# Optimization experiments

Hardware: AMD Instinct MI355X
Metric: run time of the kernel (lower is better)

Reference implementation:

```python
import jax, jax.numpy as jnp
import numpy as np

D_MODEL = 1024
NUM_HEADS = 16
D_K = D_MODEL // NUM_HEADS
B, S = 2, 2048
NEG = -1e9


def setup_inputs() -> dict:
    key = jax.random.key(0)
    ks = jax.random.split(key, 12)
    sc = 1.0 / np.sqrt(D_MODEL)
    inp = {
        'Q': jax.random.normal(ks[0], (B, S, D_MODEL), jnp.float32),
        'K': jax.random.normal(ks[1], (B, S, D_MODEL), jnp.float32),
        'V': jax.random.normal(ks[2], (B, S, D_MODEL), jnp.float32),
        # causal additive mask: 1.0 above diagonal -> scores += mask * -1e9
        'mask': jnp.triu(jnp.ones((S, S), jnp.float32), k=1),
        'Wq': jax.random.normal(ks[3], (D_MODEL, D_MODEL), jnp.float32) * sc,
        'bq': jnp.zeros((D_MODEL,), jnp.float32),
        'Wk': jax.random.normal(ks[4], (D_MODEL, D_MODEL), jnp.float32) * sc,
        'bk': jnp.zeros((D_MODEL,), jnp.float32),
        'Wv': jax.random.normal(ks[5], (D_MODEL, D_MODEL), jnp.float32) * sc,
        'bv': jnp.zeros((D_MODEL,), jnp.float32),
        'Wo': jax.random.normal(ks[6], (D_MODEL, D_MODEL), jnp.float32) * sc,
        'bo': jnp.zeros((D_MODEL,), jnp.float32),
    }
    return inp


def _split_heads(x):
    # [B,S,D] -> [B,H,S,d_k]
    b, s, _ = x.shape
    return x.reshape(b, s, NUM_HEADS, D_K).transpose(0, 2, 1, 3)


def reference(Q, K, V, mask, Wq, bq, Wk, bk, Wv, bv, Wo, bo):
    # torch Linear: y = x @ W.T + b
    q = _split_heads(Q @ Wq.T + bq)  # [B,H,S,d_k]
    k = _split_heads(K @ Wk.T + bk)
    v = _split_heads(V @ Wv.T + bv)
    scores = jnp.einsum('bhqd,bhkd->bhqk', q, k) / np.sqrt(D_K)
    scores = scores + mask * NEG  # mask broadcasts over [B,H]
    probs = jax.nn.softmax(scores, axis=-1)
    attn = jnp.einsum('bhqk,bhkd->bhqd', probs, v)  # [B,H,S,d_k]
    attn = attn.transpose(0, 2, 1, 3).reshape(Q.shape[0], Q.shape[1], D_MODEL)
    return attn @ Wo.T + bo
```

## Files before the change

kernel.cpp:

```cpp
#include <hip/hip_runtime.h>
#include <cstdint>
#include <cstddef>

#define D_MODEL 1024
#define NHEADS  16
#define DK      64
#define BATCH   2
#define SEQ     2048
#define MTOT    (BATCH*SEQ)
#define NT      (SEQ/64)

typedef unsigned short u16;
typedef __attribute__((ext_vector_type(8))) __bf16 bf16x8;
typedef __attribute__((ext_vector_type(4))) float  f32x4;
typedef __attribute__((ext_vector_type(4))) uint32_t u32x4;

static __device__ __forceinline__ u16 f2bf(float f) {
  union { float f; uint32_t u; } v; v.f = f;
  uint32_t u = v.u;
  u += 0x7fffu + ((u >> 16) & 1u);
  return (u16)(u >> 16);
}

static __device__ __forceinline__ void gload16(const void* g, void* l) {
  __builtin_amdgcn_global_load_lds((const __attribute__((address_space(1))) void*)g,
                                   (__attribute__((address_space(3))) void*)l,
                                   16, 0, 0);
}

__global__ void cast_bf16_kernel(const float* __restrict__ in, u16* __restrict__ out, int n) {
  int i = (blockIdx.x * blockDim.x + threadIdx.x) * 4;
  if (i >= n) return;
  float4 f = *reinterpret_cast<const float4*>(in + i);
  ushort4 o;
  o.x = f2bf(f.x); o.y = f2bf(f.y); o.z = f2bf(f.z); o.w = f2bf(f.w);
  *reinterpret_cast<ushort4*>(out + i) = o;
}

__global__ __launch_bounds__(256, 2) void gemm_qkv(
    const u16* __restrict__ A,
    const u16* __restrict__ W0, const u16* __restrict__ W1, const u16* __restrict__ W2,
    const float* __restrict__ b0, const float* __restrict__ b1, const float* __restrict__ b2,
    u16* __restrict__ out_q, u16* __restrict__ out_k, u16* __restrict__ out_v) {
  constexpr int K = 1024;
  __shared__ __align__(16) u16 lA[128 * 64];
  __shared__ __align__(16) u16 lB[128 * 64];
  const int w = threadIdx.x >> 6, lane = threadIdx.x & 63;
  const int blockM = blockIdx.x * 128, blockN = blockIdx.y * 128;
  const int sel = blockIdx.x >> 5;
  const u16*  Bt   = sel == 0 ? W0 : (sel == 1 ? W1 : W2);
  const float* bias = sel == 0 ? b0 : (sel == 1 ? b1 : b2);
  const int wm = (w >> 1) * 64, wn = (w & 1) * 64;
  f32x4 acc[4][4] = {};
  for (int kt = 0; kt < K; kt += 64) {
#pragma unroll
    for (int it = 0; it < 4; ++it) {
      int rowb = w * 32 + it * 8;
      int row  = rowb + (lane >> 3);
      int cc   = (lane & 7) * 8;
      gload16(A  + (size_t)(blockM + row) * K + kt + cc, &lA[rowb * 64]);
      gload16(Bt + (size_t)(blockN + row) * K + kt + cc, &lB[rowb * 64]);
    }
    __syncthreads();
#pragma unroll
    for (int kc = 0; kc < 2; ++kc) {
      bf16x8 af[4], bfr[4];
#pragma unroll
      for (int i = 0; i < 4; ++i)
        af[i] = *(const bf16x8*)&lA[(wm + i * 16 + (lane & 15)) * 64 + kc * 32 + (lane >> 4) * 8];
#pragma unroll
      for (int j = 0; j < 4; ++j)
        bfr[j] = *(const bf16x8*)&lB[(wn + j * 16 + (lane & 15)) * 64 + kc * 32 + (lane >> 4) * 8];
#pragma unroll
      for (int i = 0; i < 4; ++i)
#pragma unroll
        for (int j = 0; j < 4; ++j)
          acc[i][j] = __builtin_amdgcn_mfma_f32_16x16x32_bf16(af[i], bfr[j], acc[i][j], 0, 0, 0);
    }
    __syncthreads();
  }
  u16* outqk = sel ? out_k : out_q;
#pragma unroll
  for (int i = 0; i < 4; ++i)
#pragma unroll
    for (int j = 0; j < 4; ++j)
#pragma unroll
      for (int r = 0; r < 4; ++r) {
        int m = blockM + wm + i * 16 + (lane >> 4) * 4 + r;
        int n = blockN + wn + j * 16 + (lane & 15);
        float val = acc[i][j][r] + bias[n];
        int ml = m & (MTOT - 1);
        int b = ml >> 11, s = ml & (SEQ - 1), h = n >> 6, d = n & (DK - 1);
        u16 bv = f2bf(val);
        if (sel == 2)
          out_v[(((size_t)(b * NHEADS + h)) * DK + d) * SEQ + s] = bv;
        else
          outqk[(((size_t)(b * NHEADS + h)) * SEQ + s) * DK + d] = bv;
      }
}

__global__ __launch_bounds__(256, 2) void gemm_out(
    const u16* __restrict__ A, const u16* __restrict__ Bt,
    const float* __restrict__ bias, float* __restrict__ outp) {
  constexpr int K = 1024, N = 1024;
  __shared__ __align__(16) u16 lA[128 * 64];
  __shared__ __align__(16) u16 lB[128 * 64];
  const int w = threadIdx.x >> 6, lane = threadIdx.x & 63;
  const int blockM = blockIdx.x * 128, blockN = blockIdx.y * 128;
  const int wm = (w >> 1) * 64, wn = (w & 1) * 64;
  f32x4 acc[4][4] = {};
  for (int kt = 0; kt < K; kt += 64) {
#pragma unroll
    for (int it = 0; it < 4; ++it) {
      int rowb = w * 32 + it * 8;
      int row  = rowb + (lane >> 3);
      int cc   = (lane & 7) * 8;
      gload16(A  + (size_t)(blockM + row) * K + kt + cc, &lA[rowb * 64]);
      gload16(Bt + (size_t)(blockN + row) * K + kt + cc, &lB[rowb * 64]);
    }
    __syncthreads();
#pragma unroll
    for (int kc = 0; kc < 2; ++kc) {
      bf16x8 af[4], bfr[4];
#pragma unroll
      for (int i = 0; i < 4; ++i)
        af[i] = *(const bf16x8*)&lA[(wm + i * 16 + (lane & 15)) * 64 + kc * 32 + (lane >> 4) * 8];
#pragma unroll
      for (int j = 0; j < 4; ++j)
        bfr[j] = *(const bf16x8*)&lB[(wn + j * 16 + (lane & 15)) * 64 + kc * 32 + (lane >> 4) * 8];
#pragma unroll
      for (int i = 0; i < 4; ++i)
#pragma unroll
        for (int j = 0; j < 4; ++j)
          acc[i][j] = __builtin_amdgcn_mfma_f32_16x16x32_bf16(af[i], bfr[j], acc[i][j], 0, 0, 0);
    }
    __syncthreads();
  }
#pragma unroll
  for (int i = 0; i < 4; ++i)
#pragma unroll
    for (int j = 0; j < 4; ++j)
#pragma unroll
      for (int r = 0; r < 4; ++r) {
        int m = blockM + wm + i * 16 + (lane >> 4) * 4 + r;
        int n = blockN + wn + j * 16 + (lane & 15);
        outp[(size_t)m * N + n] = acc[i][j][r] + bias[n];
      }
}

static __device__ __forceinline__ void stage_kv(
    const u16* kp, const u16* vp, int j0,
    u16* bufK, u16* bufV, int w, int lane) {
  const int rsub = lane >> 3;
  const int cl = ((lane & 7) ^ rsub) << 3;
#pragma unroll
  for (int it = 0; it < 2; ++it) {
    const int rowb = w * 16 + it * 8;
    gload16(kp + (size_t)(j0 + rowb + rsub) * DK + cl, bufK + rowb * 64);
    gload16(vp + (size_t)(rowb + rsub) * SEQ + j0 + cl, bufV + rowb * 64);
  }
}

__global__ __launch_bounds__(256, 4) void attn_kernel(
    const u16* __restrict__ qh, const u16* __restrict__ kh,
    const u16* __restrict__ vt, u16* __restrict__ attnb) {
  __shared__ __align__(16) u16 lKV[2][2][64 * 64];
  const int w = threadIdx.x >> 6, lane = threadIdx.x & 63;
  const int g = lane >> 4, q15 = lane & 15;
  const int bh = blockIdx.y;
  const int b = bh >> 4, h = bh & 15;
  const u16* qp = qh + (size_t)bh * SEQ * DK;
  const u16* kp = kh + (size_t)bh * SEQ * DK;
  const u16* vp = vt + (size_t)bh * DK * SEQ;

  for (int pi = 0; pi < 2; ++pi) {
    const int qt = pi ? (NT - 1 - blockIdx.x) : blockIdx.x;
    const int qbase = qt * 64;
    const int qrow = qbase + w * 16 + q15;
    bf16x8 aq[2];
    const u16* qr = qp + (size_t)qrow * DK;
#pragma unroll
    for (int kc = 0; kc < 2; ++kc)
      aq[kc] = *(const bf16x8*)(qr + kc * 32 + g * 8);

    float m_run = -1e30f, l_run = 0.f;
    f32x4 oacc[4] = {};
    const int nt = qt + 1;
    __syncthreads();
    stage_kv(kp, vp, 0, lKV[0][0], lKV[0][1], w, lane);

    for (int t = 0; t < nt; ++t) {
      __syncthreads();
      const int cur = t & 1;
      if (t + 1 < nt)
        stage_kv(kp, vp, (t + 1) * 64, lKV[cur ^ 1][0], lKV[cur ^ 1][1], w, lane);
      const u16* bK = lKV[cur][0];
      const u16* bV = lKV[cur][1];

      f32x4 sacc[4] = {};
      __builtin_amdgcn_s_setprio(1);
#pragma unroll
      for (int kc = 0; kc < 2; ++kc)
#pragma unroll
        for (int nb = 0; nb < 4; ++nb) {
          const int rr = nb * 16 + q15;
          const int cc = kc * 4 + g;
          bf16x8 kf = *(const bf16x8*)&bK[rr * 64 + ((cc ^ (rr & 7)) << 3)];
          sacc[nb] = __builtin_amdgcn_mfma_f32_16x16x32_bf16(kf, aq[kc], sacc[nb], 0, 0, 0);
        }
      __builtin_amdgcn_s_setprio(0);

      const bool diag = (t == qt);
      float pv[4][4];
      float mx = -1e30f;
#pragma unroll
      for (int nb = 0; nb < 4; ++nb)
#pragma unroll
        for (int r = 0; r < 4; ++r) {
          float s = sacc[nb][r] * 0.125f;
          if (diag && (t * 64 + nb * 16 + g * 4 + r > qrow)) s = -1e30f;
          pv[nb][r] = s;
          mx = fmaxf(mx, s);
        }
      mx = fmaxf(mx, __shfl_xor(mx, 16));
      mx = fmaxf(mx, __shfl_xor(mx, 32));
      const float mn = fmaxf(m_run, mx);
      const float alpha = __expf(m_run - mn);
      m_run = mn;
      float rs = 0.f;
#pragma unroll
      for (int nb = 0; nb < 4; ++nb)
#pragma unroll
        for (int r = 0; r < 4; ++r) {
          float e = __expf(pv[nb][r] - mn);
          pv[nb][r] = e;
          rs += e;
        }
      rs += __shfl_xor(rs, 16);
      rs += __shfl_xor(rs, 32);
      l_run = l_run * alpha + rs;

      uint32_t pk[4][2];
#pragma unroll
      for (int nb = 0; nb < 4; ++nb) {
        pk[nb][0] = (uint32_t)f2bf(pv[nb][0]) | ((uint32_t)f2bf(pv[nb][1]) << 16);
        pk[nb][1] = (uint32_t)f2bf(pv[nb][2]) | ((uint32_t)f2bf(pv[nb][3]) << 16);
      }
#pragma unroll
      for (int nd = 0; nd < 4; ++nd)
#pragma unroll
        for (int r = 0; r < 4; ++r) oacc[nd][r] *= alpha;

#pragma unroll
      for (int jc = 0; jc < 2; ++jc) {
        union { u32x4 u; bf16x8 bvec; } pf;
        const int sgbase = (g & 1) * 2;
#pragma unroll
        for (int W = 0; W < 4; ++W) {
          const int src = (sgbase + (W >> 1)) * 16 + q15;
          const uint32_t lo = (uint32_t)__shfl((int)pk[2 * jc][W & 1], src, 64);
          const uint32_t hi = (uint32_t)__shfl((int)pk[2 * jc + 1][W & 1], src, 64);
          pf.u[W] = (lane >= 32) ? hi : lo;
        }
        __builtin_amdgcn_s_setprio(1);
#pragma unroll
        for (int nd = 0; nd < 4; ++nd) {
          const int rr = nd * 16 + q15;
          const int cc = jc * 4 + g;
          bf16x8 vf = *(const bf16x8*)&bV[rr * 64 + ((cc ^ (rr & 7)) << 3)];
          oacc[nd] = __builtin_amdgcn_mfma_f32_16x16x32_bf16(vf, pf.bvec, oacc[nd], 0, 0, 0);
        }
        __builtin_amdgcn_s_setprio(0);
      }
    }

    const float rl = 1.0f / l_run;
#pragma unroll
    for (int nd = 0; nd < 4; ++nd) {
      ushort4 st;
      st.x = f2bf(oacc[nd][0] * rl);
      st.y = f2bf(oacc[nd][1] * rl);
      st.z = f2bf(oacc[nd][2] * rl);
      st.w = f2bf(oacc[nd][3] * rl);
      *(ushort4*)&attnb[((size_t)(b * SEQ + qrow)) * D_MODEL + h * 64 + nd * 16 + g * 4] = st;
    }
  }
}

extern "C" void kernel_launch(void* const* d_in, const int* in_sizes, int n_in,
                              void* d_out, int out_size, void* d_ws, size_t ws_size,
                              hipStream_t stream) {
  (void)in_sizes; (void)n_in; (void)out_size; (void)ws_size;
  const float* Q  = (const float*)d_in[0];
  const float* K  = (const float*)d_in[1];
  const float* V  = (const float*)d_in[2];
  const float* Wq = (const float*)d_in[4];
  const float* bq = (const float*)d_in[5];
  const float* Wk = (const float*)d_in[6];
  const float* bk = (const float*)d_in[7];
  const float* Wv = (const float*)d_in[8];
  const float* bv = (const float*)d_in[9];
  const float* Wo = (const float*)d_in[10];
  const float* bo = (const float*)d_in[11];

  char* ws = (char*)d_ws;
  size_t off = 0;
  auto carve = [&](size_t bytes) { char* p = ws + off; off += bytes; return p; };
  const size_t szX = (size_t)MTOT * D_MODEL * 2;
  const size_t szW = (size_t)D_MODEL * D_MODEL * 2;
  u16* Qb  = (u16*)carve(szX);
  u16* Kb  = (u16*)carve(szX);
  u16* Vb  = (u16*)carve(szX);
  u16* Wqb = (u16*)carve(szW);
  u16* Wkb = (u16*)carve(szW);
  u16* Wvb = (u16*)carve(szW);
  u16* Wob = (u16*)carve(szW);
  u16* qhB = (u16*)carve(szX);
  u16* khB = (u16*)carve(szX);
  u16* vtB = (u16*)carve(szX);
  u16* attnb = Qb;

  const int nX = MTOT * D_MODEL;
  const int nW = D_MODEL * D_MODEL;
  cast_bf16_kernel<<<nX / 1024, 256, 0, stream>>>(Q,  Qb,  nX);
  cast_bf16_kernel<<<nX / 1024, 256, 0, stream>>>(K,  Kb,  nX);
  cast_bf16_kernel<<<nX / 1024, 256, 0, stream>>>(V,  Vb,  nX);
  cast_bf16_kernel<<<nW / 1024, 256, 0, stream>>>(Wq, Wqb, nW);
  cast_bf16_kernel<<<nW / 1024, 256, 0, stream>>>(Wk, Wkb, nW);
  cast_bf16_kernel<<<nW / 1024, 256, 0, stream>>>(Wv, Wvb, nW);
  cast_bf16_kernel<<<nW / 1024, 256, 0, stream>>>(Wo, Wob, nW);

  gemm_qkv<<<dim3(3 * MTOT / 128, D_MODEL / 128), 256, 0, stream>>>(
      Qb, Wqb, Wkb, Wvb, bq, bk, bv, qhB, khB, vtB);

  attn_kernel<<<dim3(NT / 2, BATCH * NHEADS), 256, 0, stream>>>(qhB, khB, vtB, attnb);

  gemm_out<<<dim3(MTOT / 128, D_MODEL / 128), 256, 0, stream>>>(attnb, Wob, bo, (float*)d_out);
}
```

Measured before the change: 147.0 us.

## Fuse casts, fold softmax scale into Q, lazy rescale, XCD-aware attention mapping

Merges the seven cast launches into one kernel and switches to the native bf16 conversion. Folds the 1/sqrt(dk)·log2e factor into the Q projection epilogue so the attention softmax can use exp2 directly. Adds a lazy online-softmax rescale that only adjusts the running max when it grows by more than a threshold. Remaps attention blocks so each XCD works on a contiguous group of heads, and halves the M tile of the output GEMM to launch more blocks. The lazy rescale and scale folding slightly change numerics and rely on bounded growth of the exponent.

```diff
diff --git a/kernel.cpp b/kernel.cpp
--- a/kernel.cpp
+++ b/kernel.cpp
@@ -15,12 +15,7 @@
 typedef __attribute__((ext_vector_type(4))) float  f32x4;
 typedef __attribute__((ext_vector_type(4))) uint32_t u32x4;
 
-static __device__ __forceinline__ u16 f2bf(float f) {
-  union { float f; uint32_t u; } v; v.f = f;
-  uint32_t u = v.u;
-  u += 0x7fffu + ((u >> 16) & 1u);
-  return (u16)(u >> 16);
-}
+#define QSCALE 0.18033688f
 
 static __device__ __forceinline__ void gload16(const void* g, void* l) {
   __builtin_amdgcn_global_load_lds((const __attribute__((address_space(1))) void*)g,
@@ -28,13 +23,30 @@
                                    16, 0, 0);
 }
 
-__global__ void cast_bf16_kernel(const float* __restrict__ in, u16* __restrict__ out, int n) {
-  int i = (blockIdx.x * blockDim.x + threadIdx.x) * 4;
-  if (i >= n) return;
-  float4 f = *reinterpret_cast<const float4*>(in + i);
-  ushort4 o;
-  o.x = f2bf(f.x); o.y = f2bf(f.y); o.z = f2bf(f.z); o.w = f2bf(f.w);
-  *reinterpret_cast<ushort4*>(out + i) = o;
+__global__ void cast_all_kernel(
+    const float* __restrict__ Q, const float* __restrict__ K, const float* __restrict__ V,
+    const float* __restrict__ Wq, const float* __restrict__ Wk,
+    const float* __restrict__ Wv, const float* __restrict__ Wo,
+    u16* __restrict__ dstX, u16* __restrict__ dstW) {
+  constexpr int NX = MTOT * D_MODEL;
+  constexpr int NW = D_MODEL * D_MODEL;
+  const int i = (blockIdx.x * blockDim.x + threadIdx.x) * 4;
+  const float* src;
+  u16* dst;
+  if (i < 3 * NX) {
+    dst = dstX + i;
+    src = (i < NX) ? Q + i : (i < 2 * NX) ? K + (i - NX) : V + (i - 2 * NX);
+  } else {
+    const int j = i - 3 * NX;
+    dst = dstW + j;
+    const int ws = j >> 20;
+    const int jo = j & (NW - 1);
+    src = (ws == 0) ? Wq + jo : (ws == 1) ? Wk + jo : (ws == 2) ? Wv + jo : Wo + jo;
+  }
+  float4 f = *reinterpret_cast<const float4*>(src);
+  union { __bf16 h[4]; ushort4 s; } o;
+  o.h[0] = (__bf16)f.x; o.h[1] = (__bf16)f.y; o.h[2] = (__bf16)f.z; o.h[3] = (__bf16)f.w;
+  *reinterpret_cast<ushort4*>(dst) = o.s;
 }
 
 __global__ __launch_bounds__(256, 2) void gemm_qkv(
@@ -89,9 +101,10 @@
         int m = blockM + wm + i * 16 + (lane >> 4) * 4 + r;
         int n = blockN + wn + j * 16 + (lane & 15);
         float val = acc[i][j][r] + bias[n];
+        if (sel == 0) val *= QSCALE;
         int ml = m & (MTOT - 1);
         int b = ml >> 11, s = ml & (SEQ - 1), h = n >> 6, d = n & (DK - 1);
-        u16 bv = f2bf(val);
+        u16 bv; { union { __bf16 h2; u16 u; } cv; cv.h2 = (__bf16)val; bv = cv.u; }
         if (sel == 2)
           out_v[(((size_t)(b * NHEADS + h)) * DK + d) * SEQ + s] = bv;
         else
@@ -103,33 +116,39 @@
     const u16* __restrict__ A, const u16* __restrict__ Bt,
     const float* __restrict__ bias, float* __restrict__ outp) {
   constexpr int K = 1024, N = 1024;
-  __shared__ __align__(16) u16 lA[128 * 64];
+  __shared__ __align__(16) u16 lA[64 * 64];
   __shared__ __align__(16) u16 lB[128 * 64];
   const int w = threadIdx.x >> 6, lane = threadIdx.x & 63;
-  const int blockM = blockIdx.x * 128, blockN = blockIdx.y * 128;
-  const int wm = (w >> 1) * 64, wn = (w & 1) * 64;
-  f32x4 acc[4][4] = {};
+  const int blockM = blockIdx.x * 64, blockN = blockIdx.y * 128;
+  const int wm = (w >> 1) * 32, wn = (w & 1) * 64;
+  f32x4 acc[2][4] = {};
   for (int kt = 0; kt < K; kt += 64) {
+#pragma unroll
+    for (int it = 0; it < 2; ++it) {
+      int rowb = w * 16 + it * 8;
+      int row  = rowb + (lane >> 3);
+      int cc   = (lane & 7) * 8;
+      gload16(A + (size_t)(blockM + row) * K + kt + cc, &lA[rowb * 64]);
+    }
 #pragma unroll
     for (int it = 0; it < 4; ++it) {
       int rowb = w * 32 + it * 8;
       int row  = rowb + (lane >> 3);
       int cc   = (lane & 7) * 8;
-      gload16(A  + (size_t)(blockM + row) * K + kt + cc, &lA[rowb * 64]);
       gload16(Bt + (size_t)(blockN + row) * K + kt + cc, &lB[rowb * 64]);
     }
     __syncthreads();
 #pragma unroll
     for (int kc = 0; kc < 2; ++kc) {
-      bf16x8 af[4], bfr[4];
-#pragma unroll
-      for (int i = 0; i < 4; ++i)
+      bf16x8 af[2], bfr[4];
+#pragma unroll
+      for (int i = 0; i < 2; ++i)
         af[i] = *(const bf16x8*)&lA[(wm + i * 16 + (lane & 15)) * 64 + kc * 32 + (lane >> 4) * 8];
 #pragma unroll
       for (int j = 0; j < 4; ++j)
         bfr[j] = *(const bf16x8*)&lB[(wn + j * 16 + (lane & 15)) * 64 + kc * 32 + (lane >> 4) * 8];
 #pragma unroll
-      for (int i = 0; i < 4; ++i)
+      for (int i = 0; i < 2; ++i)
 #pragma unroll
         for (int j = 0; j < 4; ++j)
           acc[i][j] = __builtin_amdgcn_mfma_f32_16x16x32_bf16(af[i], bfr[j], acc[i][j], 0, 0, 0);
@@ -137,7 +156,7 @@
     __syncthreads();
   }
 #pragma unroll
-  for (int i = 0; i < 4; ++i)
+  for (int i = 0; i < 2; ++i)
 #pragma unroll
     for (int j = 0; j < 4; ++j)
 #pragma unroll
@@ -167,14 +186,17 @@
   __shared__ __align__(16) u16 lKV[2][2][64 * 64];
   const int w = threadIdx.x >> 6, lane = threadIdx.x & 63;
   const int g = lane >> 4, q15 = lane & 15;
-  const int bh = blockIdx.y;
+  const int lid = blockIdx.x;
+  const int xcd = lid & 7, slot = lid >> 3;
+  const int bh  = xcd * 4 + (slot >> 4);
+  const int qtp = slot & 15;
   const int b = bh >> 4, h = bh & 15;
   const u16* qp = qh + (size_t)bh * SEQ * DK;
   const u16* kp = kh + (size_t)bh * SEQ * DK;
   const u16* vp = vt + (size_t)bh * DK * SEQ;
 
   for (int pi = 0; pi < 2; ++pi) {
-    const int qt = pi ? (NT - 1 - blockIdx.x) : blockIdx.x;
+    const int qt = pi ? (NT - 1 - qtp) : qtp;
     const int qbase = qt * 64;
     const int qrow = qbase + w * 16 + q15;
     bf16x8 aq[2];
@@ -210,46 +232,61 @@
         }
       __builtin_amdgcn_s_setprio(0);
 
-      const bool diag = (t == qt);
-      float pv[4][4];
+      float pvv[4][4];
       float mx = -1e30f;
-#pragma unroll
-      for (int nb = 0; nb < 4; ++nb)
-#pragma unroll
-        for (int r = 0; r < 4; ++r) {
-          float s = sacc[nb][r] * 0.125f;
-          if (diag && (t * 64 + nb * 16 + g * 4 + r > qrow)) s = -1e30f;
-          pv[nb][r] = s;
-          mx = fmaxf(mx, s);
-        }
+      if (t == qt) {
+#pragma unroll
+        for (int nb = 0; nb < 4; ++nb)
+#pragma unroll
+          for (int r = 0; r < 4; ++r) {
+            float s = sacc[nb][r];
+            if (t * 64 + nb * 16 + g * 4 + r > qrow) s = -1e30f;
+            pvv[nb][r] = s;
+            mx = fmaxf(mx, s);
+          }
+      } else {
+#pragma unroll
+        for (int nb = 0; nb < 4; ++nb)
+#pragma unroll
+          for (int r = 0; r < 4; ++r) {
+            float s = sacc[nb][r];
+            pvv[nb][r] = s;
+            mx = fmaxf(mx, s);
+          }
+      }
       mx = fmaxf(mx, __shfl_xor(mx, 16));
       mx = fmaxf(mx, __shfl_xor(mx, 32));
-      const float mn = fmaxf(m_run, mx);
-      const float alpha = __expf(m_run - mn);
-      m_run = mn;
+      if (__any(mx > m_run + 8.0f)) {
+        const float mn = fmaxf(m_run, mx);
+        const float alpha = __builtin_amdgcn_exp2f(m_run - mn);
+        m_run = mn;
+        l_run *= alpha;
+#pragma unroll
+        for (int nd = 0; nd < 4; ++nd)
+#pragma unroll
+          for (int r = 0; r < 4; ++r) oacc[nd][r] *= alpha;
+      }
       float rs = 0.f;
 #pragma unroll
       for (int nb = 0; nb < 4; ++nb)
 #pragma unroll
         for (int r = 0; r < 4; ++r) {
-          float e = __expf(pv[nb][r] - mn);
-          pv[nb][r] = e;
+          float e = __builtin_amdgcn_exp2f(pvv[nb][r] - m_run);
+          pvv[nb][r] = e;
           rs += e;
         }
       rs += __shfl_xor(rs, 16);
       rs += __shfl_xor(rs, 32);
-      l_run = l_run * alpha + rs;
+      l_run += rs;
 
       uint32_t pk[4][2];
 #pragma unroll
       for (int nb = 0; nb < 4; ++nb) {
-        pk[nb][0] = (uint32_t)f2bf(pv[nb][0]) | ((uint32_t)f2bf(pv[nb][1]) << 16);
-        pk[nb][1] = (uint32_t)f2bf(pv[nb][2]) | ((uint32_t)f2bf(pv[nb][3]) << 16);
-      }
-#pragma unroll
-      for (int nd = 0; nd < 4; ++nd)
-#pragma unroll
-        for (int r = 0; r < 4; ++r) oacc[nd][r] *= alpha;
+        union { __bf16 h2[2]; uint32_t u; } t0, t1;
+        t0.h2[0] = (__bf16)pvv[nb][0]; t0.h2[1] = (__bf16)pvv[nb][1];
+        t1.h2[0] = (__bf16)pvv[nb][2]; t1.h2[1] = (__bf16)pvv[nb][3];
+        pk[nb][0] = t0.u; pk[nb][1] = t1.u;
+      }
 
 #pragma unroll
       for (int jc = 0; jc < 2; ++jc) {
@@ -277,12 +314,12 @@
     const float rl = 1.0f / l_run;
 #pragma unroll
     for (int nd = 0; nd < 4; ++nd) {
-      ushort4 st;
-      st.x = f2bf(oacc[nd][0] * rl);
-      st.y = f2bf(oacc[nd][1] * rl);
-      st.z = f2bf(oacc[nd][2] * rl);
-      st.w = f2bf(oacc[nd][3] * rl);
-      *(ushort4*)&attnb[((size_t)(b * SEQ + qrow)) * D_MODEL + h * 64 + nd * 16 + g * 4] = st;
+      union { __bf16 h4[4]; ushort4 s4; } st;
+      st.h4[0] = (__bf16)(oacc[nd][0] * rl);
+      st.h4[1] = (__bf16)(oacc[nd][1] * rl);
+      st.h4[2] = (__bf16)(oacc[nd][2] * rl);
+      st.h4[3] = (__bf16)(oacc[nd][3] * rl);
+      *(ushort4*)&attnb[((size_t)(b * SEQ + qrow)) * D_MODEL + h * 64 + nd * 16 + g * 4] = st.s4;
     }
   }
 }
@@ -319,21 +356,15 @@
   u16* khB = (u16*)carve(szX);
   u16* vtB = (u16*)carve(szX);
   u16* attnb = Qb;
-
-  const int nX = MTOT * D_MODEL;
-  const int nW = D_MODEL * D_MODEL;
-  cast_bf16_kernel<<<nX / 1024, 256, 0, stream>>>(Q,  Qb,  nX);
-  cast_bf16_kernel<<<nX / 1024, 256, 0, stream>>>(K,  Kb,  nX);
-  cast_bf16_kernel<<<nX / 1024, 256, 0, stream>>>(V,  Vb,  nX);
-  cast_bf16_kernel<<<nW / 1024, 256, 0, stream>>>(Wq, Wqb, nW);
-  cast_bf16_kernel<<<nW / 1024, 256, 0, stream>>>(Wk, Wkb, nW);
-  cast_bf16_kernel<<<nW / 1024, 256, 0, stream>>>(Wv, Wvb, nW);
-  cast_bf16_kernel<<<nW / 1024, 256, 0, stream>>>(Wo, Wob, nW);
+  (void)Kb; (void)Vb; (void)Wkb; (void)Wvb; (void)Wob;
+
+  const int nTot = 3 * MTOT * D_MODEL + 4 * D_MODEL * D_MODEL;
+  cast_all_kernel<<<nTot / 1024, 256, 0, stream>>>(Q, K, V, Wq, Wk, Wv, Wo, Qb, Wqb);
 
   gemm_qkv<<<dim3(3 * MTOT / 128, D_MODEL / 128), 256, 0, stream>>>(
       Qb, Wqb, Wkb, Wvb, bq, bk, bv, qhB, khB, vtB);
 
-  attn_kernel<<<dim3(NT / 2, BATCH * NHEADS), 256, 0, stream>>>(qhB, khB, vtB, attnb);
-
-  gemm_out<<<dim3(MTOT / 128, D_MODEL / 128), 256, 0, stream>>>(attnb, Wob, bo, (float*)d_out);
-}
+  attn_kernel<<<(NT / 2) * BATCH * NHEADS, 256, 0, stream>>>(qhB, khB, vtB, attnb);
+
+  gemm_out<<<dim3(MTOT / 64, D_MODEL / 128), 256, 0, stream>>>(attnb, Wob, bo, (float*)d_out);
+}
```

Measured after the change: 128.9 us. -12.3%, faster.
